# Performance work log

Measured on AMD Instinct MI355X. Metric: run time of the kernel, lower is better.

## Reference

```python
import jax, jax.numpy as jnp
import numpy as np

TEMP = 0.5  # temperature_f from init


def setup_inputs() -> dict:
    key = jax.random.key(0)
    k1, k2, k3 = jax.random.split(key, 3)
    B, d = 4096, 128
    h_i = jax.random.normal(k1, (B, d), dtype=jnp.float32)
    h_j = jax.random.normal(k2, (B, d), dtype=jnp.float32)
    S = jax.random.uniform(k3, (B, B), dtype=jnp.float32)
    return {"h_i": h_i, "h_j": h_j, "S": S}


def reference(h_i, h_j, S):
    B = h_i.shape[0]
    N = 2 * B
    h = jnp.concatenate([h_i, h_j], axis=0)                 # [N, d]
    sim = jnp.matmul(h, h.T) / TEMP                          # [N, N]
    # S_2 = 1 - (S**2).repeat(2,2); sim1 = sim * S_2
    S2 = 1.0 - jnp.tile(S * S, (2, 2))                       # [N, N]
    sim1 = sim * S2
    # positives: diag(sim, +B) and diag(sim, -B)
    idx = jnp.arange(B)
    pos = jnp.concatenate([sim[idx, idx + B], sim[idx + B, idx]])  # [N]
    # negatives mask: exclude diagonal and the positive-pair positions
    i = jnp.arange(N)[:, None]
    j = jnp.arange(N)[None, :]
    neg_mask = ~((i == j) | (j == (i + B) % N))              # [N, N], N-2 True per row
    neg = jnp.where(neg_mask, sim1, -jnp.inf)                # masked entries drop out of logsumexp
    # CrossEntropy(label=0, reduction='sum') over logits=[pos, negatives]:
    # loss_n = logsumexp(logits_n) - pos_n  (order of negatives is irrelevant)
    logits = jnp.concatenate([pos[:, None], neg], axis=1)    # [N, N-1] effective
    lse = jax.nn.logsumexp(logits, axis=1)
    loss = jnp.sum(lse - pos) / N
    return loss
```

## Files before the change

### kernel.cpp

```cpp
#include <hip/hip_runtime.h>
#include <hip/hip_bf16.h>

#define B_ROWS 4096
#define NN     8192
#define DD     128
#define NSPLIT 64
#define NTRI   2080
#define SPA    68
#define CSHIFT 128.0f

typedef __attribute__((ext_vector_type(8))) short s8v;
typedef __attribute__((ext_vector_type(4))) float f4v;
typedef __attribute__((ext_vector_type(2))) float f2v;
typedef __attribute__((ext_vector_type(4))) unsigned short u16x4;
typedef unsigned int u32;

static constexpr float SCALE_H = 1.6986436f;
static constexpr float SCALE2  = 2.8853900818f;
static constexpr float LN2     = 0.6931471805599453f;

__device__ __forceinline__ float fast_exp2(float x) {
#if __has_builtin(__builtin_amdgcn_exp2f)
    return __builtin_amdgcn_exp2f(x);
#else
    return exp2f(x);
#endif
}

__device__ __forceinline__ unsigned short s2m_pack(float x, bool msk) {
    float s2 = msk ? 0.f : 1.f - x * x;
    union { __hip_bfloat16 h; unsigned short u; } cv;
    cv.h = __float2bfloat16(s2);
    return cv.u;
}

__device__ __forceinline__ float bf16f(unsigned short u) {
    return __uint_as_float(((u32)u) << 16);
}

typedef __attribute__((address_space(1))) const u32 gu32;
typedef __attribute__((address_space(3))) u32 lu32;
__device__ __forceinline__ void gload_lds16(const void* g, void* l) {
    __builtin_amdgcn_global_load_lds((gu32*)g, (lu32*)l, 16, 0, 0);
}

__global__ void hpos_kernel(const float* __restrict__ hi, const float* __restrict__ hj,
                            __hip_bfloat16* __restrict__ hb, float* __restrict__ pos2) {
    int w = threadIdx.x >> 6, l = threadIdx.x & 63;
    int row = blockIdx.x * 4 + w;
    f2v a = ((const f2v*)(hi + (size_t)row * DD))[l];
    f2v b = ((const f2v*)(hj + (size_t)row * DD))[l];
    float d = a[0] * b[0] + a[1] * b[1];
    #pragma unroll
    for (int off = 32; off; off >>= 1) d += __shfl_xor(d, off, 64);
    if (l == 0) pos2[row] = SCALE2 * d;
    union { ushort2 u2; __hip_bfloat16 h[2]; } ua, ub;
    ua.h[0] = __float2bfloat16(a[0] * SCALE_H);
    ua.h[1] = __float2bfloat16(a[1] * SCALE_H);
    ub.h[0] = __float2bfloat16(b[0] * SCALE_H);
    ub.h[1] = __float2bfloat16(b[1] * SCALE_H);
    ((ushort2*)(hb + (size_t)row * DD))[l] = ua.u2;
    ((ushort2*)(hb + (size_t)(row + B_ROWS) * DD))[l] = ub.u2;
}

__global__ __launch_bounds__(512, 4)
void main_kernel(const __hip_bfloat16* __restrict__ hb, const float* __restrict__ S,
                 float* __restrict__ ssplit) {
    __shared__ short ldsB[128][128];

    const int orig = blockIdx.x;
    const int bid  = (orig & 7) * (NTRI / 8) + (orig >> 3);
    int j = (int)((sqrtf(8.0f * (float)bid + 1.0f) - 1.0f) * 0.5f);
    while (((j + 1) * (j + 2)) / 2 <= bid) ++j;
    while ((j * (j + 1)) / 2 > bid) --j;
    const int i = bid - (j * (j + 1)) / 2;
    const bool diag = (i == j);

    const int tid = threadIdx.x;
    const int l  = tid & 63;
    const int w  = tid >> 6;
    const int wm = w >> 1, wn = w & 1;
    const int lc = l & 15;
    const int lk = l >> 4;
    const int r64 = i * 64, c64 = j * 64;

    const s8v* hb8 = (const s8v*)hb;

    #pragma unroll
    for (int i2 = 0; i2 < 4; i2++) {
        const int rowb = w * 16 + i2 * 4;
        const int lrw  = rowb + lk;
        const int grow = c64 + ((lrw < 64) ? lrw : (lrw - 64 + B_ROWS));
        const int sc16 = lc ^ (lrw & 7);
        gload_lds16((const char*)hb + ((size_t)grow << 8) + (sc16 << 4),
                    (char*)&ldsB[rowb][0]);
    }

    const int prr = tid >> 3;
    const int pc8 = (tid & 7) * 8;
    f4v a0, a1, b0, b1;
    {
        const float* gA = S + (size_t)(r64 + prr) * B_ROWS + c64 + pc8;
        const float* gB = S + (size_t)(c64 + prr) * B_ROWS + r64 + pc8;
        a0 = ((const f4v*)gA)[0]; a1 = ((const f4v*)gA)[1];
        b0 = ((const f4v*)gB)[0]; b1 = ((const f4v*)gB)[1];
    }

    s8v afr[2][4];
    #pragma unroll
    for (int fm = 0; fm < 2; fm++) {
        int ar = (r64 + wm * 16 + lc) + fm * B_ROWS;
        #pragma unroll
        for (int kk = 0; kk < 4; kk++)
            afr[fm][kk] = hb8[ar * 16 + kk * 4 + lk];
    }

    asm volatile("" : "+v"(a0), "+v"(a1), "+v"(b0), "+v"(b1) :: "memory");

    __syncthreads();

    const char* bp[4];
    {
        const char* bb = (const char*)ldsB + (wn * 32 + lc) * 256;
        #pragma unroll
        for (int kk = 0; kk < 4; kk++)
            bp[kk] = bb + (((kk * 4 + lk) ^ (lc & 7)) << 4);
    }
    f4v acc[2][2][2];
    #pragma unroll
    for (int fm = 0; fm < 2; fm++)
        #pragma unroll
        for (int fh = 0; fh < 2; fh++)
            #pragma unroll
            for (int cg = 0; cg < 2; cg++) acc[fm][fh][cg] = f4v{0.f, 0.f, 0.f, 0.f};
    #pragma unroll
    for (int kk = 0; kk < 4; kk++) {
        #pragma unroll
        for (int fh = 0; fh < 2; fh++)
            #pragma unroll
            for (int cg = 0; cg < 2; cg++) {
                s8v bf = *(const s8v*)(bp[kk] + fh * 16384 + cg * 4096);
                acc[0][fh][cg] = __builtin_amdgcn_mfma_f32_16x16x32_bf16(
                    afr[0][kk], bf, acc[0][fh][cg], 0, 0, 0);
                acc[1][fh][cg] = __builtin_amdgcn_mfma_f32_16x16x32_bf16(
                    afr[1][kk], bf, acc[1][fh][cg], 0, 0, 0);
            }
    }

    __syncthreads();

    unsigned short* sAp = (unsigned short*)&ldsB[0][0];
    unsigned short* sBp = sAp + 64 * SPA;
    {
        u16x4 pa0, pa1, pb0, pb1;
        #pragma unroll
        for (int e = 0; e < 4; e++) {
            pa0[e] = s2m_pack(a0[e], diag && (pc8 + e     == prr));
            pa1[e] = s2m_pack(a1[e], diag && (pc8 + 4 + e == prr));
            pb0[e] = s2m_pack(b0[e], false);
            pb1[e] = s2m_pack(b1[e], false);
        }
        *(u16x4*)&sAp[prr * SPA + pc8]     = pa0;
        *(u16x4*)&sAp[prr * SPA + pc8 + 4] = pa1;
        *(u16x4*)&sBp[prr * SPA + pc8]     = pb0;
        *(u16x4*)&sBp[prr * SPA + pc8 + 4] = pb1;
    }
    __syncthreads();

    float rsum[2][4], csum[2][2];
    #pragma unroll
    for (int fm = 0; fm < 2; fm++)
        #pragma unroll
        for (int r = 0; r < 4; r++) rsum[fm][r] = 0.f;
    csum[0][0] = csum[0][1] = csum[1][0] = csum[1][1] = 0.f;

    #pragma unroll
    for (int r = 0; r < 4; r++) {
        const int rr = wm * 16 + lk * 4 + r;
        #pragma unroll
        for (int cg = 0; cg < 2; cg++) {
            const int cc = wn * 32 + cg * 16 + lc;
            const float s2a = bf16f(sAp[rr * SPA + cc]);
            const float s2b = bf16f(sBp[cc * SPA + rr]);
            #pragma unroll
            for (int fm = 0; fm < 2; fm++)
                #pragma unroll
                for (int fh = 0; fh < 2; fh++) {
                    const float a = acc[fm][fh][cg][r];
                    rsum[fm][r]  += fast_exp2(fmaf(a, s2a, -CSHIFT));
                    csum[fh][cg] += fast_exp2(fmaf(a, s2b, -CSHIFT));
                }
        }
    }

    float* mrg = (float*)((char*)&ldsB[0][0] + 2 * 64 * SPA * 2);
    #pragma unroll
    for (int fm = 0; fm < 2; fm++) {
        #pragma unroll
        for (int r = 0; r < 4; r++) {
            float ss = rsum[fm][r];
            #pragma unroll
            for (int off = 1; off < 16; off <<= 1) ss += __shfl_xor(ss, off, 64);
            if (lc == 0) mrg[wn * 128 + fm * 64 + (wm * 16 + lk * 4 + r)] = ss;
        }
    }
    #pragma unroll
    for (int fh = 0; fh < 2; fh++) {
        #pragma unroll
        for (int cg = 0; cg < 2; cg++) {
            float ss = csum[fh][cg];
            ss += __shfl_xor(ss, 16, 64);
            ss += __shfl_xor(ss, 32, 64);
            if (l < 16) mrg[256 + wm * 128 + fh * 64 + (wn * 32 + cg * 16 + lc)] = ss;
        }
    }
    __syncthreads();

    if (tid < 128) {
        int fm = tid >> 6, rho = tid & 63;
        float v = mrg[fm * 64 + rho] + mrg[128 + fm * 64 + rho];
        ssplit[(size_t)j * NN + (r64 + rho + fm * B_ROWS)] = v;
    } else if (!diag && tid < 256) {
        int t2 = tid - 128, fh = t2 >> 6, cc = t2 & 63;
        float v = mrg[256 +   0 + fh * 64 + cc] + mrg[256 + 128 + fh * 64 + cc]
                + mrg[256 + 256 + fh * 64 + cc] + mrg[256 + 384 + fh * 64 + cc];
        ssplit[(size_t)i * NN + (c64 + cc + fh * B_ROWS)] = v;
    }
}

__global__ __launch_bounds__(256)
void reduce_kernel(const float* __restrict__ ssplit, const float* __restrict__ pos2,
                   float* __restrict__ partial) {
    __shared__ float red[256];
    const int n = blockIdx.x * 256 + threadIdx.x;
    float p = pos2[n & (B_ROWS - 1)];
    float Ssum = fast_exp2(p - CSHIFT);
    #pragma unroll 8
    for (int sp = 0; sp < NSPLIT; sp++)
        Ssum += ssplit[(size_t)sp * NN + n];
    red[threadIdx.x] = (CSHIFT + log2f(Ssum)) - p;
    __syncthreads();
    for (int st = 128; st; st >>= 1) {
        if (threadIdx.x < st) red[threadIdx.x] += red[threadIdx.x + st];
        __syncthreads();
    }
    if (threadIdx.x == 0) partial[blockIdx.x] = red[0];
}

__global__ void final_kernel(const float* __restrict__ partial, float* __restrict__ out) {
    if (threadIdx.x == 0) {
        float s = 0.f;
        #pragma unroll
        for (int i = 0; i < 32; i++) s += partial[i];
        out[0] = s * (LN2 / (float)NN);
    }
}

extern "C" void kernel_launch(void* const* d_in, const int* in_sizes, int n_in,
                              void* d_out, int out_size, void* d_ws, size_t ws_size,
                              hipStream_t stream) {
    (void)in_sizes; (void)n_in; (void)out_size; (void)ws_size;
    const float* hi = (const float*)d_in[0];
    const float* hj = (const float*)d_in[1];
    const float* S  = (const float*)d_in[2];

    char* ws = (char*)d_ws;
    __hip_bfloat16* hb = (__hip_bfloat16*)ws;
    float* pos2   = (float*)(ws + 2097152);
    float* ssplit = (float*)(ws + 2097152 + 16384);
    float* partial= (float*)(ws + 2097152 + 16384 + 2097152);

    hpos_kernel<<<1024, 256, 0, stream>>>(hi, hj, hb, pos2);
    main_kernel<<<NTRI, 512, 0, stream>>>(hb, S, ssplit);
    reduce_kernel<<<32, 256, 0, stream>>>(ssplit, pos2, partial);
    final_kernel<<<1, 64, 0, stream>>>(partial, (float*)d_out);
}
```

Baseline: 50.97 us.

## Quantize S mask to u8 in dedicated LDS, drop block syncs, write bf16 per-wave partials

Converts the 1-S^2 weights to 8-bit fixed point and stores them, with B already transposed, in separate LDS arrays before the matmul, so the two post-MFMA barriers and the LDS reuse go away. Each wave now writes its own bf16 row and column partial sums straight to global memory instead of merging them through LDS. The reduce kernel then sums more, narrower partials and skips the unused triangular slots. This trades accuracy (8-bit weights, bf16 partials) and a larger reduce workload for less synchronization in the main kernel, and the byte-wise transposed LDS stores may cause bank conflicts.

After: 102.5 us. +101.0%, slower.

```diff
diff --git a/kernel.cpp b/kernel.cpp
--- a/kernel.cpp
+++ b/kernel.cpp
@@ -4,20 +4,20 @@
 #define B_ROWS 4096
 #define NN     8192
 #define DD     128
-#define NSPLIT 64
 #define NTRI   2080
-#define SPA    68
 #define CSHIFT 128.0f
 
 typedef __attribute__((ext_vector_type(8))) short s8v;
 typedef __attribute__((ext_vector_type(4))) float f4v;
 typedef __attribute__((ext_vector_type(2))) float f2v;
-typedef __attribute__((ext_vector_type(4))) unsigned short u16x4;
 typedef unsigned int u32;
+typedef unsigned short u16;
+typedef unsigned char u8;
 
 static constexpr float SCALE_H = 1.6986436f;
 static constexpr float SCALE2  = 2.8853900818f;
 static constexpr float LN2     = 0.6931471805599453f;
+static constexpr float INV255  = 1.0f / 255.0f;
 
 __device__ __forceinline__ float fast_exp2(float x) {
 #if __has_builtin(__builtin_amdgcn_exp2f)
@@ -27,14 +27,18 @@
 #endif
 }
 
-__device__ __forceinline__ unsigned short s2m_pack(float x, bool msk) {
+__device__ __forceinline__ u8 s2m_pack8(float x, bool msk) {
     float s2 = msk ? 0.f : 1.f - x * x;
-    union { __hip_bfloat16 h; unsigned short u; } cv;
-    cv.h = __float2bfloat16(s2);
+    return (u8)(s2 * 255.f + 0.5f);
+}
+
+__device__ __forceinline__ u16 f2bf(float x) {
+    union { __hip_bfloat16 h; u16 u; } cv;
+    cv.h = __float2bfloat16(x);
     return cv.u;
 }
 
-__device__ __forceinline__ float bf16f(unsigned short u) {
+__device__ __forceinline__ float bf2f(u16 u) {
     return __uint_as_float(((u32)u) << 16);
 }
 
@@ -65,8 +69,10 @@
 
 __global__ __launch_bounds__(512, 4)
 void main_kernel(const __hip_bfloat16* __restrict__ hb, const float* __restrict__ S,
-                 float* __restrict__ ssplit) {
+                 u16* __restrict__ ssr, u16* __restrict__ ssc) {
     __shared__ short ldsB[128][128];
+    __shared__ __align__(16) u8 sAu[64 * 64];
+    __shared__ __align__(16) u8 sBtu[64 * 64];
 
     const int orig = blockIdx.x;
     const int bid  = (orig & 7) * (NTRI / 8) + (orig >> 3);
@@ -96,14 +102,26 @@
                     (char*)&ldsB[rowb][0]);
     }
 
-    const int prr = tid >> 3;
-    const int pc8 = (tid & 7) * 8;
-    f4v a0, a1, b0, b1;
     {
+        const int prr = tid >> 3;
+        const int pc8 = (tid & 7) * 8;
         const float* gA = S + (size_t)(r64 + prr) * B_ROWS + c64 + pc8;
         const float* gB = S + (size_t)(c64 + prr) * B_ROWS + r64 + pc8;
-        a0 = ((const f4v*)gA)[0]; a1 = ((const f4v*)gA)[1];
-        b0 = ((const f4v*)gB)[0]; b1 = ((const f4v*)gB)[1];
+        f4v a0 = ((const f4v*)gA)[0], a1 = ((const f4v*)gA)[1];
+        f4v b0 = ((const f4v*)gB)[0], b1 = ((const f4v*)gB)[1];
+        union { u8 c[8]; uint2 v; } qa;
+        u8 qb[8];
+        #pragma unroll
+        for (int e = 0; e < 4; e++) {
+            qa.c[e]     = s2m_pack8(a0[e], diag && (pc8 + e     == prr));
+            qa.c[e + 4] = s2m_pack8(a1[e], diag && (pc8 + 4 + e == prr));
+            qb[e]     = s2m_pack8(b0[e], false);
+            qb[e + 4] = s2m_pack8(b1[e], false);
+        }
+        *(uint2*)&sAu[prr * 64 + pc8] = qa.v;
+        #pragma unroll
+        for (int e = 0; e < 8; e++)
+            sBtu[(pc8 + e) * 64 + prr] = qb[e];
     }
 
     s8v afr[2][4];
@@ -114,9 +132,6 @@
         for (int kk = 0; kk < 4; kk++)
             afr[fm][kk] = hb8[ar * 16 + kk * 4 + lk];
     }
-
-    asm volatile("" : "+v"(a0), "+v"(a1), "+v"(b0), "+v"(b1) :: "memory");
-
     __syncthreads();
 
     const char* bp[4];
@@ -147,26 +162,6 @@
             }
     }
 
-    __syncthreads();
-
-    unsigned short* sAp = (unsigned short*)&ldsB[0][0];
-    unsigned short* sBp = sAp + 64 * SPA;
-    {
-        u16x4 pa0, pa1, pb0, pb1;
-        #pragma unroll
-        for (int e = 0; e < 4; e++) {
-            pa0[e] = s2m_pack(a0[e], diag && (pc8 + e     == prr));
-            pa1[e] = s2m_pack(a1[e], diag && (pc8 + 4 + e == prr));
-            pb0[e] = s2m_pack(b0[e], false);
-            pb1[e] = s2m_pack(b1[e], false);
-        }
-        *(u16x4*)&sAp[prr * SPA + pc8]     = pa0;
-        *(u16x4*)&sAp[prr * SPA + pc8 + 4] = pa1;
-        *(u16x4*)&sBp[prr * SPA + pc8]     = pb0;
-        *(u16x4*)&sBp[prr * SPA + pc8 + 4] = pb1;
-    }
-    __syncthreads();
-
     float rsum[2][4], csum[2][2];
     #pragma unroll
     for (int fm = 0; fm < 2; fm++)
@@ -180,8 +175,8 @@
         #pragma unroll
         for (int cg = 0; cg < 2; cg++) {
             const int cc = wn * 32 + cg * 16 + lc;
-            const float s2a = bf16f(sAp[rr * SPA + cc]);
-            const float s2b = bf16f(sBp[cc * SPA + rr]);
+            const float s2a = (float)sAu[rr * 64 + cc] * INV255;
+            const float s2b = (float)sBtu[rr * 64 + cc] * INV255;
             #pragma unroll
             for (int fm = 0; fm < 2; fm++)
                 #pragma unroll
@@ -193,7 +188,6 @@
         }
     }
 
-    float* mrg = (float*)((char*)&ldsB[0][0] + 2 * 64 * SPA * 2);
     #pragma unroll
     for (int fm = 0; fm < 2; fm++) {
         #pragma unroll
@@ -201,7 +195,10 @@
             float ss = rsum[fm][r];
             #pragma unroll
             for (int off = 1; off < 16; off <<= 1) ss += __shfl_xor(ss, off, 64);
-            if (lc == 0) mrg[wn * 128 + fm * 64 + (wm * 16 + lk * 4 + r)] = ss;
+            if (lc == 0) {
+                int rho = wm * 16 + lk * 4 + r;
+                ssr[(size_t)(j * 2 + wn) * NN + (r64 + rho + fm * B_ROWS)] = f2bf(ss);
+            }
         }
     }
     #pragma unroll
@@ -211,33 +208,26 @@
             float ss = csum[fh][cg];
             ss += __shfl_xor(ss, 16, 64);
             ss += __shfl_xor(ss, 32, 64);
-            if (l < 16) mrg[256 + wm * 128 + fh * 64 + (wn * 32 + cg * 16 + lc)] = ss;
-        }
-    }
-    __syncthreads();
-
-    if (tid < 128) {
-        int fm = tid >> 6, rho = tid & 63;
-        float v = mrg[fm * 64 + rho] + mrg[128 + fm * 64 + rho];
-        ssplit[(size_t)j * NN + (r64 + rho + fm * B_ROWS)] = v;
-    } else if (!diag && tid < 256) {
-        int t2 = tid - 128, fh = t2 >> 6, cc = t2 & 63;
-        float v = mrg[256 +   0 + fh * 64 + cc] + mrg[256 + 128 + fh * 64 + cc]
-                + mrg[256 + 256 + fh * 64 + cc] + mrg[256 + 384 + fh * 64 + cc];
-        ssplit[(size_t)i * NN + (c64 + cc + fh * B_ROWS)] = v;
+            if (l < 16) {
+                int cc = wn * 32 + cg * 16 + lc;
+                ssc[(size_t)(i * 4 + wm) * NN + (c64 + cc + fh * B_ROWS)] = f2bf(ss);
+            }
+        }
     }
 }
 
 __global__ __launch_bounds__(256)
-void reduce_kernel(const float* __restrict__ ssplit, const float* __restrict__ pos2,
-                   float* __restrict__ partial) {
+void reduce_kernel(const u16* __restrict__ ssr, const u16* __restrict__ ssc,
+                   const float* __restrict__ pos2, float* __restrict__ partial) {
     __shared__ float red[256];
     const int n = blockIdx.x * 256 + threadIdx.x;
+    const int it = (n & (B_ROWS - 1)) >> 6;
     float p = pos2[n & (B_ROWS - 1)];
     float Ssum = fast_exp2(p - CSHIFT);
-    #pragma unroll 8
-    for (int sp = 0; sp < NSPLIT; sp++)
-        Ssum += ssplit[(size_t)sp * NN + n];
+    for (int sp = 2 * it; sp < 128; sp++)
+        Ssum += bf2f(ssr[(size_t)sp * NN + n]);
+    for (int sp = 0; sp < 4 * it; sp++)
+        Ssum += bf2f(ssc[(size_t)sp * NN + n]);
     red[threadIdx.x] = (CSHIFT + log2f(Ssum)) - p;
     __syncthreads();
     for (int st = 128; st; st >>= 1) {
@@ -267,11 +257,12 @@
     char* ws = (char*)d_ws;
     __hip_bfloat16* hb = (__hip_bfloat16*)ws;
     float* pos2   = (float*)(ws + 2097152);
-    float* ssplit = (float*)(ws + 2097152 + 16384);
-    float* partial= (float*)(ws + 2097152 + 16384 + 2097152);
+    u16*   ssr    = (u16*)(ws + 2097152 + 16384);
+    u16*   ssc    = (u16*)(ws + 2097152 + 16384 + 2097152);
+    float* partial= (float*)(ws + 2097152 + 16384 + 2097152 + 4194304);
 
     hpos_kernel<<<1024, 256, 0, stream>>>(hi, hj, hb, pos2);
-    main_kernel<<<NTRI, 512, 0, stream>>>(hb, S, ssplit);
-    reduce_kernel<<<32, 256, 0, stream>>>(ssplit, pos2, partial);
+    main_kernel<<<NTRI, 512, 0, stream>>>(hb, S, ssr, ssc);
+    reduce_kernel<<<32, 256, 0, stream>>>(ssr, ssc, pos2, partial);
     final_kernel<<<1, 64, 0, stream>>>(partial, (float*)d_out);
 }
```
